# Optimization experiments

Hardware: AMD Instinct MI355X
Metric: run time of the kernel (lower is better)

## Reference

```python
import jax, jax.numpy as jnp
import numpy as np

B, C, H, W = 4, 256, 64, 64
DQK = C // 8  # 32


def setup_inputs() -> dict:
    key = jax.random.key(0)
    ks = jax.random.split(key, 8)
    s = 0.02
    return {
        "x": jax.random.normal(ks[0], (B, C, H, W), dtype=jnp.float32),
        "Wq": jax.random.normal(ks[1], (DQK, C), dtype=jnp.float32) * s,
        "bq": jnp.zeros((DQK,), dtype=jnp.float32),
        "Wk": jax.random.normal(ks[2], (DQK, C), dtype=jnp.float32) * s,
        "bk": jnp.zeros((DQK,), dtype=jnp.float32),
        "Wv": jax.random.normal(ks[3], (C, C), dtype=jnp.float32) * s,
        "bv": jnp.zeros((C,), dtype=jnp.float32),
        "gamma": jax.random.normal(ks[4], (1,), dtype=jnp.float32) * 0.1,
    }


def reference(x, Wq, bq, Wk, bk, Wv, bv, gamma):
    b, c, h, w = x.shape
    n = h * w
    xf = x.reshape(b, c, n)  # [B, C, N]
    # 1x1 convs == per-pixel linear projections
    q = jnp.einsum('dc,bcn->bdn', Wq, xf) + bq[None, :, None]  # [B, C/8, N]
    k = jnp.einsum('dc,bcn->bdn', Wk, xf) + bk[None, :, None]  # [B, C/8, N]
    v = jnp.einsum('dc,bcn->bdn', Wv, xf) + bv[None, :, None]  # [B, C, N]
    # attn[b, i, j] = softmax_j( q_i . k_j / sqrt(C) )
    scores = jnp.einsum('bdn,bdm->bnm', q, k) / (c ** 0.5)  # [B, N, N]
    attn = jax.nn.softmax(scores, axis=-1)
    # out = v @ attn^T : out[b, c, i] = sum_j v[b, c, j] * attn[b, i, j]
    out = jnp.einsum('bcj,bij->bci', v, attn)  # [B, C, N]
    return (gamma * out + xf).reshape(b, c, h, w)
```

## Files before the change

kernel.cpp:

```cpp
#include <hip/hip_runtime.h>

#define NN 4096
#define CC 256
#define DQ 32
#define NB 4

typedef float        f32x4  __attribute__((ext_vector_type(4)));
typedef float        f32x16 __attribute__((ext_vector_type(16)));
typedef short        s16x4  __attribute__((ext_vector_type(4)));
typedef short        s16x8  __attribute__((ext_vector_type(8)));
typedef unsigned int u32x2  __attribute__((ext_vector_type(2)));
typedef unsigned int u32x4  __attribute__((ext_vector_type(4)));

__device__ __forceinline__ unsigned short f2bf(float f) {
  unsigned u = __builtin_bit_cast(unsigned, f);
  u += 0x7fffu + ((u >> 16) & 1u);
  return (unsigned short)(u >> 16);
}

__device__ __forceinline__ f32x4 mfma16(s16x4 a, s16x4 b, f32x4 c) {
  return __builtin_amdgcn_mfma_f32_16x16x16bf16_1k(a, b, c, 0, 0, 0);
}
__device__ __forceinline__ f32x16 mfma32b(s16x8 a, s16x8 b, f32x16 c) {
  return __builtin_amdgcn_mfma_f32_32x32x16_bf16(a, b, c, 0, 0, 0);
}

__device__ __forceinline__ s16x4 lo4(u32x4 r) { u32x2 t = {r[0], r[1]}; return __builtin_bit_cast(s16x4, t); }
__device__ __forceinline__ s16x4 hi4(u32x4 r) { u32x2 t = {r[2], r[3]}; return __builtin_bit_cast(s16x4, t); }
__device__ __forceinline__ s16x8 bc8(u32x4 r) { return __builtin_bit_cast(s16x8, r); }

__device__ __forceinline__ float fexp2(float x) {
  float r;
  asm("v_exp_f32 %0, %1" : "=v"(r) : "v"(x));
  return r;
}

#define XLS 264

__global__ __launch_bounds__(256)
void proj_kernel(const float* __restrict__ x,
                 const float* __restrict__ Wq, const float* __restrict__ bq,
                 const float* __restrict__ Wk, const float* __restrict__ bk,
                 const float* __restrict__ Wv, const float* __restrict__ bv,
                 unsigned short* __restrict__ QT,
                 unsigned short* __restrict__ KT,
                 unsigned short* __restrict__ Vm) {
  __shared__ unsigned short Xl[64 * XLS];
  const int tid = threadIdx.x;
  const int b   = blockIdx.y;
  const int n0  = blockIdx.x * 64;

  {
    const int n4 = (tid & 15) * 4;
    int c = tid >> 4;
    const float* xp = x + (size_t)(b * CC + c) * NN + n0 + n4;
    #pragma unroll
    for (int it = 0; it < 16; ++it) {
      f32x4 v = *reinterpret_cast<const f32x4*>(xp);
      #pragma unroll
      for (int e = 0; e < 4; ++e)
        Xl[(n4 + e) * XLS + c] = f2bf(v[e]);
      c += 16; xp += (size_t)16 * NN;
    }
  }
  __syncthreads();

  const int wave = tid >> 6;
  const int lane = tid & 63;
  const int l16  = lane & 15;
  const int g    = lane >> 4;
  const float qscale = 0.0901684400555602f;

  const float* wrowp[5];
  float wsc[5];
  #pragma unroll
  for (int rt = 0; rt < 5; ++rt) {
    const int R0 = (wave * 5 + rt) * 16;
    const int R  = R0 + l16;
    if (R0 < 32)      { wrowp[rt] = Wq + R * CC;        wsc[rt] = qscale; }
    else if (R0 < 64) { wrowp[rt] = Wk + (R - 32) * CC; wsc[rt] = 1.0f; }
    else              { wrowp[rt] = Wv + (R - 64) * CC; wsc[rt] = 1.0f; }
  }

  f32x4 acc[5][4];
  #pragma unroll
  for (int rt = 0; rt < 5; ++rt)
    #pragma unroll
    for (int nt = 0; nt < 4; ++nt) acc[rt][nt] = (f32x4){0.f, 0.f, 0.f, 0.f};

  for (int k0 = 0; k0 < CC; k0 += 32) {
    s16x4 xb[4][2];
    #pragma unroll
    for (int nt = 0; nt < 4; ++nt) {
      const unsigned short* p = &Xl[(l16 + 16 * nt) * XLS + k0 + 8 * g];
      u32x4 raw = *reinterpret_cast<const u32x4*>(p);
      xb[nt][0] = lo4(raw);
      xb[nt][1] = hi4(raw);
    }
    #pragma unroll
    for (int rt = 0; rt < 5; ++rt) {
      const float* wp = wrowp[rt] + k0 + 8 * g;
      f32x4 w0 = *reinterpret_cast<const f32x4*>(wp);
      f32x4 w1 = *reinterpret_cast<const f32x4*>(wp + 4);
      const float sc = wsc[rt];
      s16x4 wa0, wa1;
      #pragma unroll
      for (int e = 0; e < 4; ++e) {
        wa0[e] = (short)f2bf(w0[e] * sc);
        wa1[e] = (short)f2bf(w1[e] * sc);
      }
      #pragma unroll
      for (int nt = 0; nt < 4; ++nt) {
        acc[rt][nt] = mfma16(wa0, xb[nt][0], acc[rt][nt]);
        acc[rt][nt] = mfma16(wa1, xb[nt][1], acc[rt][nt]);
      }
    }
  }

  #pragma unroll
  for (int rt = 0; rt < 5; ++rt) {
    const int R0 = (wave * 5 + rt) * 16;
    float bias_r[4];
    {
      const float* bp; float bsc;
      if (R0 < 32)      { bp = bq + R0;      bsc = qscale; }
      else if (R0 < 64) { bp = bk + R0 - 32; bsc = 1.0f; }
      else              { bp = bv + R0 - 64; bsc = 1.0f; }
      #pragma unroll
      for (int r = 0; r < 4; ++r) bias_r[r] = bp[4 * g + r] * bsc;
    }
    #pragma unroll
    for (int nt = 0; nt < 4; ++nt) {
      const int n = n0 + nt * 16 + l16;
      float v0 = acc[rt][nt][0] + bias_r[0];
      float v1 = acc[rt][nt][1] + bias_r[1];
      float v2 = acc[rt][nt][2] + bias_r[2];
      float v3 = acc[rt][nt][3] + bias_r[3];
      if (R0 < 32) {
        u32x2 pk = { (unsigned)f2bf(v0) | ((unsigned)f2bf(v1) << 16),
                     (unsigned)f2bf(v2) | ((unsigned)f2bf(v3) << 16) };
        unsigned short* dst = QT + ((size_t)b * NN + n) * DQ + R0 + 4 * g;
        *reinterpret_cast<u32x2*>(dst) = pk;
      } else if (R0 < 64) {
        const int d0     = R0 - 32 + 4 * g;
        const int kh     = d0 >> 4;
        const int g2v    = (d0 >> 3) & 1;
        const int e0     = d0 & 7;
        const int jt     = n >> 5;
        const int lane_t = (n & 31) + 32 * g2v;
        u32x2 pk = { (unsigned)f2bf(v0) | ((unsigned)f2bf(v1) << 16),
                     (unsigned)f2bf(v2) | ((unsigned)f2bf(v3) << 16) };
        unsigned short* kd = KT + (((size_t)(b * 128 + jt) * 2 + kh) * 64 + lane_t) * 8 + e0;
        *reinterpret_cast<u32x2*>(kd) = pk;
      } else {
        const int c0  = R0 - 64 + 4 * g;
        const int cq  = c0 >> 5;
        const int cl  = c0 & 31;
        const int jt  = (n0 + nt * 16) >> 5;
        const int kh  = nt & 1;
        const int g2v = (l16 >> 2) & 1;
        const int e   = (l16 & 3) | (((l16 >> 3) & 1) << 2);
        unsigned short* vd = Vm
          + ((((size_t)(b * 128 + jt) * 8 + cq) * 2 + kh) * 64 + (cl + 32 * g2v)) * 8 + e;
        vd[0]  = f2bf(v0);
        vd[8]  = f2bf(v1);
        vd[16] = f2bf(v2);
        vd[24] = f2bf(v3);
      }
    }
  }
}


#define SM16(SS, L, P0, P1) { \
  const float p0=fexp2(SS[0]),  p1=fexp2(SS[1]),  p2=fexp2(SS[2]),  p3=fexp2(SS[3]); \
  const float p4=fexp2(SS[4]),  p5=fexp2(SS[5]),  p6=fexp2(SS[6]),  p7=fexp2(SS[7]); \
  const float p8=fexp2(SS[8]),  p9=fexp2(SS[9]),  pa=fexp2(SS[10]), pb=fexp2(SS[11]); \
  const float pc=fexp2(SS[12]), pd=fexp2(SS[13]), pe=fexp2(SS[14]), pf=fexp2(SS[15]); \
  L += (((p0+p1)+(p2+p3)) + ((p4+p5)+(p6+p7))) + (((p8+p9)+(pa+pb)) + ((pc+pd)+(pe+pf))); \
  unsigned q0,q1,q2,q3,q4,q5,q6,q7; \
  asm("v_cvt_pk_bf16_f32 %0, %1, %2" : "=v"(q0) : "v"(p0), "v"(p1)); \
  asm("v_cvt_pk_bf16_f32 %0, %1, %2" : "=v"(q1) : "v"(p2), "v"(p3)); \
  asm("v_cvt_pk_bf16_f32 %0, %1, %2" : "=v"(q2) : "v"(p4), "v"(p5)); \
  asm("v_cvt_pk_bf16_f32 %0, %1, %2" : "=v"(q3) : "v"(p6), "v"(p7)); \
  asm("v_cvt_pk_bf16_f32 %0, %1, %2" : "=v"(q4) : "v"(p8), "v"(p9)); \
  asm("v_cvt_pk_bf16_f32 %0, %1, %2" : "=v"(q5) : "v"(pa), "v"(pb)); \
  asm("v_cvt_pk_bf16_f32 %0, %1, %2" : "=v"(q6) : "v"(pc), "v"(pd)); \
  asm("v_cvt_pk_bf16_f32 %0, %1, %2" : "=v"(q7) : "v"(pe), "v"(pf)); \
  u32x4 _w0 = {q0,q1,q2,q3}, _w1 = {q4,q5,q6,q7}; \
  P0 = bc8(_w0); P1 = bc8(_w1); }

#define LOADSET_IMPL(T, KA, KB, V00, V01, V10, V11) { \
  { const size_t _o = (size_t)(T) * 1024; \
    KA = *(const u32x4*)(Kb + _o); \
    KB = *(const u32x4*)(Kb + _o + 512); } \
  { const size_t _o = (size_t)(T) * 8192; \
    V00 = *(const u32x4*)(Vb + _o); \
    V01 = *(const u32x4*)(Vb + _o + 512); \
    V10 = *(const u32x4*)(Vb + _o + 1024); \
    V11 = *(const u32x4*)(Vb + _o + 1536); } }
#define LOADSET(T, SET) LOADSET_IMPL(T, SET)

#define ITER_IMPL(TN, KA, KB, V00, V01, V10, V11, KAN, KBN, V00N, V01N, V10N, V11N) { \
  LOADSET_IMPL(TN, KAN, KBN, V00N, V01N, V10N, V11N); \
  f32x16 ss0 = mfma32b(bc8(KA), qf00, zz16); \
  ss0 = mfma32b(bc8(KB), qf01, ss0); \
  f32x16 ss1 = mfma32b(bc8(KA), qf10, zz16); \
  ss1 = mfma32b(bc8(KB), qf11, ss1); \
  s16x8 P00, P01, P10, P11; \
  SM16(ss0, l0, P00, P01); \
  SM16(ss1, l1, P10, P11); \
  o00 = mfma32b(bc8(V00), P00, o00); \
  o00 = mfma32b(bc8(V01), P01, o00); \
  o01 = mfma32b(bc8(V10), P00, o01); \
  o01 = mfma32b(bc8(V11), P01, o01); \
  o10 = mfma32b(bc8(V00), P10, o10); \
  o10 = mfma32b(bc8(V01), P11, o10); \
  o11 = mfma32b(bc8(V10), P10, o11); \
  o11 = mfma32b(bc8(V11), P11, o11); \
}
#define ITER(TN, SETC, SETN) ITER_IMPL(TN, SETC, SETN)

#define SET_A kA0, kB0, v000, v010, v100, v110
#define SET_B kA1, kB1, v001, v011, v101, v111
#define SET_C kA2, kB2, v002, v012, v102, v112

__global__ __launch_bounds__(512, 2)
void attn_kernel(const unsigned short* __restrict__ QT,
                 const unsigned short* __restrict__ KT,
                 const unsigned short* __restrict__ Vm,
                 const float* __restrict__ x,
                 const float* __restrict__ gamma,
                 float* __restrict__ out) {
  extern __shared__ float fb[];

  const int tid  = threadIdx.x;
  const int wave = tid >> 6;
  const int lane = tid & 63;
  const int l31  = lane & 31;
  const int g2   = lane >> 5;
  const int jq   = wave >> 2;
  const int cs   = wave & 3;

  const int gid = blockIdx.x;
  const int rr  = gid & 7;
  const int qq  = gid >> 3;
  const int b   = rr >> 1;
  const int xt  = (qq << 1) | (rr & 1);
  const int ibase = xt * 64;
  const float gamma0 = gamma[0];

  const unsigned short* Qb = QT + ((size_t)b * NN + ibase + l31) * DQ;
  const s16x8 qf00 = bc8(*(const u32x4*)(Qb + 8 * g2));
  const s16x8 qf01 = bc8(*(const u32x4*)(Qb + 16 + 8 * g2));
  const s16x8 qf10 = bc8(*(const u32x4*)(Qb + 32 * DQ + 8 * g2));
  const s16x8 qf11 = bc8(*(const u32x4*)(Qb + 32 * DQ + 16 + 8 * g2));

  f32x16 o00, o01, o10, o11, zz16;
  #pragma unroll
  for (int r = 0; r < 16; ++r) { o00[r] = 0.f; o01[r] = 0.f; o10[r] = 0.f; o11[r] = 0.f; zz16[r] = 0.f; }
  float l0 = 0.f, l1 = 0.f;

  const unsigned short* Kb = KT + (size_t)(b * 128 + jq * 64) * 1024 + lane * 8;
  const unsigned short* Vb = Vm + ((size_t)(b * 128 + jq * 64) * 8 + cs * 2) * 1024 + lane * 8;

  u32x4 kA0, kB0, v000, v010, v100, v110;
  u32x4 kA1, kB1, v001, v011, v101, v111;
  u32x4 kA2, kB2, v002, v012, v102, v112;

  LOADSET(0, SET_A);
  LOADSET(1, SET_B);

  #pragma unroll 1
  for (int tt = 0; tt < 21; ++tt) {
    const int t = 3 * tt;
    ITER(t + 2, SET_A, SET_C);
    ITER(t + 3, SET_B, SET_A);
    { const int t4 = (t + 4 < 64) ? t + 4 : 63;
      ITER(t4, SET_C, SET_B); }
  }
  ITER(63, SET_A, SET_C);

  l0 += __shfl_xor(l0, 32);
  l1 += __shfl_xor(l1, 32);

  f32x16 w0, w1; float lw;
  if (jq == 0) { w0 = o10; w1 = o11; lw = l1; }
  else         { w0 = o00; w1 = o01; lw = l0; }
  const int sW = 1 - jq;
  #pragma unroll
  for (int r = 0; r < 16; ++r) {
    fb[(((sW * 4 + cs) * 2 + 0) * 16 + r) * 64 + lane] = w0[r];
    fb[(((sW * 4 + cs) * 2 + 1) * 16 + r) * 64 + lane] = w1[r];
  }
  if (cs == 0 && g2 == 0) fb[16384 + sW * 32 + l31] = lw;
  __syncthreads();

  f32x16 m0v, m1v; float lme;
  if (jq == 0) { m0v = o00; m1v = o01; lme = l0; }
  else         { m0v = o10; m1v = o11; lme = l1; }
  const float ltot = lme + fb[16384 + jq * 32 + l31];
  const float ga = gamma0 / ltot;
  const int i = ibase + jq * 32 + l31;

  #pragma unroll
  for (int r = 0; r < 16; ++r) {
    const int c0r = cs * 64 + (r & 3) + 8 * (r >> 2) + 4 * g2;
    {
      const float part = fb[(((jq * 4 + cs) * 2 + 0) * 16 + r) * 64 + lane];
      const size_t adr = ((size_t)b * CC + c0r) * NN + i;
      out[adr] = ga * (m0v[r] + part) + x[adr];
    }
    {
      const float part = fb[(((jq * 4 + cs) * 2 + 1) * 16 + r) * 64 + lane];
      const size_t adr = ((size_t)b * CC + c0r + 32) * NN + i;
      out[adr] = ga * (m1v[r] + part) + x[adr];
    }
  }
}

extern "C" void kernel_launch(void* const* d_in, const int* in_sizes, int n_in,
                              void* d_out, int out_size, void* d_ws, size_t ws_size,
                              hipStream_t stream) {
  const float* x     = (const float*)d_in[0];
  const float* Wq    = (const float*)d_in[1];
  const float* bq    = (const float*)d_in[2];
  const float* Wk    = (const float*)d_in[3];
  const float* bk    = (const float*)d_in[4];
  const float* Wv    = (const float*)d_in[5];
  const float* bv    = (const float*)d_in[6];
  const float* gamma = (const float*)d_in[7];
  float* out = (float*)d_out;

  unsigned short* QT = (unsigned short*)d_ws;
  unsigned short* KT = QT + (size_t)NB * NN * DQ;
  unsigned short* Vm = KT + (size_t)NB * NN * DQ;

  const int ldsB = (16384 + 64) * 4;
  static bool attr_set = false;
  if (!attr_set) {
    hipFuncSetAttribute((const void*)attn_kernel,
                        hipFuncAttributeMaxDynamicSharedMemorySize, ldsB);
    attr_set = true;
  }

  dim3 gridP(64, NB), blkP(256);
  proj_kernel<<<gridP, blkP, 0, stream>>>(x, Wq, bq, Wk, bk, Wv, bv, QT, KT, Vm);
  attn_kernel<<<256, 512, ldsB, stream>>>(QT, KT, Vm, x, gamma, out);
}
```

Before: 80.57 us.

## Remap waves to one query slab each and compute row sums via MFMA

Each wave now handles a single 32-query slab and a 128-channel half of V, where before it handled both slabs and a 64-channel quarter. This halves the QK score MFMAs and exps per wave but doubles the V loads per wave. Softmax row sums now come from MFMA against a ones vector, replacing the scalar adds. The pipeline drops from triple to double buffering and occupancy is no longer pinned at 2 blocks via launch bounds, so register pressure from 16 accumulator registers per output plus 20 load registers may reduce occupancy.

```diff
diff --git a/kernel.cpp b/kernel.cpp
--- a/kernel.cpp
+++ b/kernel.cpp
@@ -172,12 +172,11 @@
 }
 
 
-#define SM16(SS, L, P0, P1) { \
+#define SM16(SS, P0, P1) { \
   const float p0=fexp2(SS[0]),  p1=fexp2(SS[1]),  p2=fexp2(SS[2]),  p3=fexp2(SS[3]); \
   const float p4=fexp2(SS[4]),  p5=fexp2(SS[5]),  p6=fexp2(SS[6]),  p7=fexp2(SS[7]); \
   const float p8=fexp2(SS[8]),  p9=fexp2(SS[9]),  pa=fexp2(SS[10]), pb=fexp2(SS[11]); \
   const float pc=fexp2(SS[12]), pd=fexp2(SS[13]), pe=fexp2(SS[14]), pf=fexp2(SS[15]); \
-  L += (((p0+p1)+(p2+p3)) + ((p4+p5)+(p6+p7))) + (((p8+p9)+(pa+pb)) + ((pc+pd)+(pe+pf))); \
   unsigned q0,q1,q2,q3,q4,q5,q6,q7; \
   asm("v_cvt_pk_bf16_f32 %0, %1, %2" : "=v"(q0) : "v"(p0), "v"(p1)); \
   asm("v_cvt_pk_bf16_f32 %0, %1, %2" : "=v"(q1) : "v"(p2), "v"(p3)); \
@@ -190,42 +189,45 @@
   u32x4 _w0 = {q0,q1,q2,q3}, _w1 = {q4,q5,q6,q7}; \
   P0 = bc8(_w0); P1 = bc8(_w1); }
 
-#define LOADSET_IMPL(T, KA, KB, V00, V01, V10, V11) { \
+#define LOADSET_IMPL(T, KA, KB, V0, V1, V2, V3, V4, V5, V6, V7) { \
   { const size_t _o = (size_t)(T) * 1024; \
     KA = *(const u32x4*)(Kb + _o); \
     KB = *(const u32x4*)(Kb + _o + 512); } \
   { const size_t _o = (size_t)(T) * 8192; \
-    V00 = *(const u32x4*)(Vb + _o); \
-    V01 = *(const u32x4*)(Vb + _o + 512); \
-    V10 = *(const u32x4*)(Vb + _o + 1024); \
-    V11 = *(const u32x4*)(Vb + _o + 1536); } }
+    V0 = *(const u32x4*)(Vb + _o); \
+    V1 = *(const u32x4*)(Vb + _o + 512); \
+    V2 = *(const u32x4*)(Vb + _o + 1024); \
+    V3 = *(const u32x4*)(Vb + _o + 1536); \
+    V4 = *(const u32x4*)(Vb + _o + 2048); \
+    V5 = *(const u32x4*)(Vb + _o + 2560); \
+    V6 = *(const u32x4*)(Vb + _o + 3072); \
+    V7 = *(const u32x4*)(Vb + _o + 3584); } }
 #define LOADSET(T, SET) LOADSET_IMPL(T, SET)
 
-#define ITER_IMPL(TN, KA, KB, V00, V01, V10, V11, KAN, KBN, V00N, V01N, V10N, V11N) { \
-  LOADSET_IMPL(TN, KAN, KBN, V00N, V01N, V10N, V11N); \
-  f32x16 ss0 = mfma32b(bc8(KA), qf00, zz16); \
-  ss0 = mfma32b(bc8(KB), qf01, ss0); \
-  f32x16 ss1 = mfma32b(bc8(KA), qf10, zz16); \
-  ss1 = mfma32b(bc8(KB), qf11, ss1); \
-  s16x8 P00, P01, P10, P11; \
-  SM16(ss0, l0, P00, P01); \
-  SM16(ss1, l1, P10, P11); \
-  o00 = mfma32b(bc8(V00), P00, o00); \
-  o00 = mfma32b(bc8(V01), P01, o00); \
-  o01 = mfma32b(bc8(V10), P00, o01); \
-  o01 = mfma32b(bc8(V11), P01, o01); \
-  o10 = mfma32b(bc8(V00), P10, o10); \
-  o10 = mfma32b(bc8(V01), P11, o10); \
-  o11 = mfma32b(bc8(V10), P10, o11); \
-  o11 = mfma32b(bc8(V11), P11, o11); \
+#define ITER_IMPL(TN, KA, KB, V0, V1, V2, V3, V4, V5, V6, V7, \
+                      KAN, KBN, V0N, V1N, V2N, V3N, V4N, V5N, V6N, V7N) { \
+  LOADSET_IMPL(TN, KAN, KBN, V0N, V1N, V2N, V3N, V4N, V5N, V6N, V7N); \
+  f32x16 ss = mfma32b(bc8(KA), qf0, zz16); \
+  ss = mfma32b(bc8(KB), qf1, ss); \
+  s16x8 P0, P1; \
+  SM16(ss, P0, P1); \
+  lacc = mfma32b(ones8, P0, lacc); \
+  lacc = mfma32b(ones8, P1, lacc); \
+  o0 = mfma32b(bc8(V0), P0, o0); \
+  o0 = mfma32b(bc8(V1), P1, o0); \
+  o1 = mfma32b(bc8(V2), P0, o1); \
+  o1 = mfma32b(bc8(V3), P1, o1); \
+  o2 = mfma32b(bc8(V4), P0, o2); \
+  o2 = mfma32b(bc8(V5), P1, o2); \
+  o3 = mfma32b(bc8(V6), P0, o3); \
+  o3 = mfma32b(bc8(V7), P1, o3); \
 }
 #define ITER(TN, SETC, SETN) ITER_IMPL(TN, SETC, SETN)
 
-#define SET_A kA0, kB0, v000, v010, v100, v110
-#define SET_B kA1, kB1, v001, v011, v101, v111
-#define SET_C kA2, kB2, v002, v012, v102, v112
-
-__global__ __launch_bounds__(512, 2)
+#define SET_A kA0, kB0, vA0, vA1, vA2, vA3, vA4, vA5, vA6, vA7
+#define SET_B kA1, kB1, vB0, vB1, vB2, vB3, vB4, vB5, vB6, vB7
+
+__global__ __launch_bounds__(512)
 void attn_kernel(const unsigned short* __restrict__ QT,
                  const unsigned short* __restrict__ KT,
                  const unsigned short* __restrict__ Vm,
@@ -240,7 +242,8 @@
   const int l31  = lane & 31;
   const int g2   = lane >> 5;
   const int jq   = wave >> 2;
-  const int cs   = wave & 3;
+  const int s    = (wave >> 1) & 1;
+  const int chv  = wave & 1;
 
   const int gid = blockIdx.x;
   const int rr  = gid & 7;
@@ -250,71 +253,65 @@
   const int ibase = xt * 64;
   const float gamma0 = gamma[0];
 
-  const unsigned short* Qb = QT + ((size_t)b * NN + ibase + l31) * DQ;
-  const s16x8 qf00 = bc8(*(const u32x4*)(Qb + 8 * g2));
-  const s16x8 qf01 = bc8(*(const u32x4*)(Qb + 16 + 8 * g2));
-  const s16x8 qf10 = bc8(*(const u32x4*)(Qb + 32 * DQ + 8 * g2));
-  const s16x8 qf11 = bc8(*(const u32x4*)(Qb + 32 * DQ + 16 + 8 * g2));
-
-  f32x16 o00, o01, o10, o11, zz16;
-  #pragma unroll
-  for (int r = 0; r < 16; ++r) { o00[r] = 0.f; o01[r] = 0.f; o10[r] = 0.f; o11[r] = 0.f; zz16[r] = 0.f; }
-  float l0 = 0.f, l1 = 0.f;
-
-  const unsigned short* Kb = KT + (size_t)(b * 128 + jq * 64) * 1024 + lane * 8;
-  const unsigned short* Vb = Vm + ((size_t)(b * 128 + jq * 64) * 8 + cs * 2) * 1024 + lane * 8;
-
-  u32x4 kA0, kB0, v000, v010, v100, v110;
-  u32x4 kA1, kB1, v001, v011, v101, v111;
-  u32x4 kA2, kB2, v002, v012, v102, v112;
-
-  LOADSET(0, SET_A);
-  LOADSET(1, SET_B);
-
-  #pragma unroll 1
-  for (int tt = 0; tt < 21; ++tt) {
-    const int t = 3 * tt;
-    ITER(t + 2, SET_A, SET_C);
-    ITER(t + 3, SET_B, SET_A);
-    { const int t4 = (t + 4 < 64) ? t + 4 : 63;
-      ITER(t4, SET_C, SET_B); }
-  }
-  ITER(63, SET_A, SET_C);
-
-  l0 += __shfl_xor(l0, 32);
-  l1 += __shfl_xor(l1, 32);
-
-  f32x16 w0, w1; float lw;
-  if (jq == 0) { w0 = o10; w1 = o11; lw = l1; }
-  else         { w0 = o00; w1 = o01; lw = l0; }
-  const int sW = 1 - jq;
+  const unsigned short* Qb = QT + ((size_t)b * NN + ibase + s * 32 + l31) * DQ;
+  const s16x8 qf0 = bc8(*(const u32x4*)(Qb + 8 * g2));
+  const s16x8 qf1 = bc8(*(const u32x4*)(Qb + 16 + 8 * g2));
+
+  const unsigned _one2 = 0x3F803F80u;
+  u32x4 _ones = {_one2, _one2, _one2, _one2};
+  const s16x8 ones8 = bc8(_ones);
+
+  f32x16 o0, o1, o2, o3, lacc, zz16;
   #pragma unroll
   for (int r = 0; r < 16; ++r) {
-    fb[(((sW * 4 + cs) * 2 + 0) * 16 + r) * 64 + lane] = w0[r];
-    fb[(((sW * 4 + cs) * 2 + 1) * 16 + r) * 64 + lane] = w1[r];
-  }
-  if (cs == 0 && g2 == 0) fb[16384 + sW * 32 + l31] = lw;
+    o0[r] = 0.f; o1[r] = 0.f; o2[r] = 0.f; o3[r] = 0.f; lacc[r] = 0.f; zz16[r] = 0.f;
+  }
+
+  const unsigned short* Kb = KT + (size_t)(b * 128 + jq * 64) * 1024 + lane * 8;
+  const unsigned short* Vb = Vm + ((size_t)(b * 128 + jq * 64) * 8 + chv * 4) * 1024 + lane * 8;
+
+  u32x4 kA0, kB0, vA0, vA1, vA2, vA3, vA4, vA5, vA6, vA7;
+  u32x4 kA1, kB1, vB0, vB1, vB2, vB3, vB4, vB5, vB6, vB7;
+
+  LOADSET(0, SET_A);
+
+  #pragma unroll 1
+  for (int tt = 0; tt < 32; ++tt) {
+    const int t0 = 2 * tt;
+    ITER(t0 + 1, SET_A, SET_B);
+    { const int t2 = (t0 + 2 < 64) ? t0 + 2 : 63;
+      ITER(t2, SET_B, SET_A); }
+  }
+
+  float l = lacc[0];
+  l += __shfl_xor(l, 32);
+
+  const int slot = s * 2 + chv;
+  if (jq == 1) {
+    #pragma unroll
+    for (int r = 0; r < 16; ++r) {
+      fb[((slot * 4 + 0) * 16 + r) * 64 + lane] = o0[r];
+      fb[((slot * 4 + 1) * 16 + r) * 64 + lane] = o1[r];
+      fb[((slot * 4 + 2) * 16 + r) * 64 + lane] = o2[r];
+      fb[((slot * 4 + 3) * 16 + r) * 64 + lane] = o3[r];
+    }
+    if (chv == 0 && g2 == 0) fb[16384 + s * 32 + l31] = l;
+  }
   __syncthreads();
-
-  f32x16 m0v, m1v; float lme;
-  if (jq == 0) { m0v = o00; m1v = o01; lme = l0; }
-  else         { m0v = o10; m1v = o11; lme = l1; }
-  const float ltot = lme + fb[16384 + jq * 32 + l31];
-  const float ga = gamma0 / ltot;
-  const int i = ibase + jq * 32 + l31;
-
-  #pragma unroll
-  for (int r = 0; r < 16; ++r) {
-    const int c0r = cs * 64 + (r & 3) + 8 * (r >> 2) + 4 * g2;
-    {
-      const float part = fb[(((jq * 4 + cs) * 2 + 0) * 16 + r) * 64 + lane];
-      const size_t adr = ((size_t)b * CC + c0r) * NN + i;
-      out[adr] = ga * (m0v[r] + part) + x[adr];
-    }
-    {
-      const float part = fb[(((jq * 4 + cs) * 2 + 1) * 16 + r) * 64 + lane];
-      const size_t adr = ((size_t)b * CC + c0r + 32) * NN + i;
-      out[adr] = ga * (m1v[r] + part) + x[adr];
+  if (jq == 0) {
+    const float lB = fb[16384 + s * 32 + l31];
+    const float ga = gamma0 / (l + lB);
+    const int i = ibase + s * 32 + l31;
+    #pragma unroll
+    for (int ct = 0; ct < 4; ++ct) {
+      const f32x16* op = (ct == 0) ? &o0 : (ct == 1) ? &o1 : (ct == 2) ? &o2 : &o3;
+      #pragma unroll
+      for (int r = 0; r < 16; ++r) {
+        const float oB = fb[((slot * 4 + ct) * 16 + r) * 64 + lane];
+        const int   c  = chv * 128 + ct * 32 + (r & 3) + 8 * (r >> 2) + 4 * g2;
+        const size_t adr = ((size_t)b * CC + c) * NN + i;
+        out[adr] = ga * ((*op)[r] + oB) + x[adr];
+      }
     }
   }
 }
```

New measurement: 202.5 us. 151% more time.

## Drop split-key reduction: each wave covers all keys, remove LDS combine

Applied to the files above, without the earlier changes.

Each block previously used 8 waves split into two key halves, whose partial outputs and row sums were merged through LDS with a barrier. Now each block has 4 waves that each loop over all 128 key tiles, so the LDS exchange, the barrier and the dynamic shared memory setup all go away. The cost is half as many waves per block and a serial loop twice as long per wave. This lowers occupancy and the latency hiding that came from running the key halves in parallel.

```diff
diff --git a/kernel.cpp b/kernel.cpp
--- a/kernel.cpp
+++ b/kernel.cpp
@@ -225,22 +225,18 @@
 #define SET_B kA1, kB1, v001, v011, v101, v111
 #define SET_C kA2, kB2, v002, v012, v102, v112
 
-__global__ __launch_bounds__(512, 2)
+__global__ __launch_bounds__(256, 1)
 void attn_kernel(const unsigned short* __restrict__ QT,
                  const unsigned short* __restrict__ KT,
                  const unsigned short* __restrict__ Vm,
                  const float* __restrict__ x,
                  const float* __restrict__ gamma,
                  float* __restrict__ out) {
-  extern __shared__ float fb[];
-
   const int tid  = threadIdx.x;
-  const int wave = tid >> 6;
+  const int cs   = tid >> 6;
   const int lane = tid & 63;
   const int l31  = lane & 31;
   const int g2   = lane >> 5;
-  const int jq   = wave >> 2;
-  const int cs   = wave & 3;
 
   const int gid = blockIdx.x;
   const int rr  = gid & 7;
@@ -261,8 +257,8 @@
   for (int r = 0; r < 16; ++r) { o00[r] = 0.f; o01[r] = 0.f; o10[r] = 0.f; o11[r] = 0.f; zz16[r] = 0.f; }
   float l0 = 0.f, l1 = 0.f;
 
-  const unsigned short* Kb = KT + (size_t)(b * 128 + jq * 64) * 1024 + lane * 8;
-  const unsigned short* Vb = Vm + ((size_t)(b * 128 + jq * 64) * 8 + cs * 2) * 1024 + lane * 8;
+  const unsigned short* Kb = KT + (size_t)b * 128 * 1024 + lane * 8;
+  const unsigned short* Vb = Vm + ((size_t)b * 128 * 8 + cs * 2) * 1024 + lane * 8;
 
   u32x4 kA0, kB0, v000, v010, v100, v110;
   u32x4 kA1, kB1, v001, v011, v101, v111;
@@ -272,49 +268,43 @@
   LOADSET(1, SET_B);
 
   #pragma unroll 1
-  for (int tt = 0; tt < 21; ++tt) {
+  for (int tt = 0; tt < 42; ++tt) {
     const int t = 3 * tt;
     ITER(t + 2, SET_A, SET_C);
     ITER(t + 3, SET_B, SET_A);
-    { const int t4 = (t + 4 < 64) ? t + 4 : 63;
+    { const int t4 = (t + 4 < 128) ? t + 4 : 127;
       ITER(t4, SET_C, SET_B); }
   }
-  ITER(63, SET_A, SET_C);
+  ITER(127, SET_A, SET_C);
+  ITER(127, SET_B, SET_A);
 
   l0 += __shfl_xor(l0, 32);
   l1 += __shfl_xor(l1, 32);
-
-  f32x16 w0, w1; float lw;
-  if (jq == 0) { w0 = o10; w1 = o11; lw = l1; }
-  else         { w0 = o00; w1 = o01; lw = l0; }
-  const int sW = 1 - jq;
+  const float ga0 = gamma0 / l0;
+  const float ga1 = gamma0 / l1;
+
+  const int i0 = ibase + l31;
+  const int i1 = ibase + 32 + l31;
   #pragma unroll
   for (int r = 0; r < 16; ++r) {
-    fb[(((sW * 4 + cs) * 2 + 0) * 16 + r) * 64 + lane] = w0[r];
-    fb[(((sW * 4 + cs) * 2 + 1) * 16 + r) * 64 + lane] = w1[r];
-  }
-  if (cs == 0 && g2 == 0) fb[16384 + sW * 32 + l31] = lw;
-  __syncthreads();
-
-  f32x16 m0v, m1v; float lme;
-  if (jq == 0) { m0v = o00; m1v = o01; lme = l0; }
-  else         { m0v = o10; m1v = o11; lme = l1; }
-  const float ltot = lme + fb[16384 + jq * 32 + l31];
-  const float ga = gamma0 / ltot;
-  const int i = ibase + jq * 32 + l31;
-
-  #pragma unroll
-  for (int r = 0; r < 16; ++r) {
-    const int c0r = cs * 64 + (r & 3) + 8 * (r >> 2) + 4 * g2;
-    {
-      const float part = fb[(((jq * 4 + cs) * 2 + 0) * 16 + r) * 64 + lane];
-      const size_t adr = ((size_t)b * CC + c0r) * NN + i;
-      out[adr] = ga * (m0v[r] + part) + x[adr];
-    }
-    {
-      const float part = fb[(((jq * 4 + cs) * 2 + 1) * 16 + r) * 64 + lane];
-      const size_t adr = ((size_t)b * CC + c0r + 32) * NN + i;
-      out[adr] = ga * (m1v[r] + part) + x[adr];
+    const int row = (r & 3) + 8 * (r >> 2) + 4 * g2;
+    const int c0  = cs * 64 + row;
+    const int c1  = cs * 64 + 32 + row;
+    {
+      const size_t a = ((size_t)b * CC + c0) * NN + i0;
+      out[a] = ga0 * o00[r] + x[a];
+    }
+    {
+      const size_t a = ((size_t)b * CC + c1) * NN + i0;
+      out[a] = ga0 * o01[r] + x[a];
+    }
+    {
+      const size_t a = ((size_t)b * CC + c0) * NN + i1;
+      out[a] = ga1 * o10[r] + x[a];
+    }
+    {
+      const size_t a = ((size_t)b * CC + c1) * NN + i1;
+      out[a] = ga1 * o11[r] + x[a];
     }
   }
 }
@@ -336,15 +326,7 @@
   unsigned short* KT = QT + (size_t)NB * NN * DQ;
   unsigned short* Vm = KT + (size_t)NB * NN * DQ;
 
-  const int ldsB = (16384 + 64) * 4;
-  static bool attr_set = false;
-  if (!attr_set) {
-    hipFuncSetAttribute((const void*)attn_kernel,
-                        hipFuncAttributeMaxDynamicSharedMemorySize, ldsB);
-    attr_set = true;
-  }
-
   dim3 gridP(64, NB), blkP(256);
   proj_kernel<<<gridP, blkP, 0, stream>>>(x, Wq, bq, Wk, bk, Wv, bv, QT, KT, Vm);
-  attn_kernel<<<256, 512, ldsB, stream>>>(QT, KT, Vm, x, gamma, out);
-}
+  attn_kernel<<<256, 256, 0, stream>>>(QT, KT, Vm, x, gamma, out);
+}
```

Result: slower. 95.11 us (+18.0%).
